# Kernel tuning notes

Hardware: AMD Instinct MI355X
Metric: run time of the kernel (lower is better)

Reference implementation:

```python
import jax, jax.numpy as jnp
import numpy as np

HIDDEN = 2048
HEAD_DIM = 128
N_HEADS = 16
N_KV_HEADS = 8
Q_DIM = N_HEADS * HEAD_DIM          # 2048
K_DIM = N_KV_HEADS * HEAD_DIM       # 1024
ROPE_THETA = 1.0e6
EPS = 1e-6
T = 4096


def setup_inputs() -> dict:
    key = jax.random.key(0)
    ks = jax.random.split(key, 4)
    x = jax.random.normal(ks[0], (T, HIDDEN), dtype=jnp.float32)
    qkv_w = jax.random.normal(ks[1], (Q_DIM + 2 * K_DIM, HIDDEN), dtype=jnp.float32) * 0.02
    o_w = jax.random.normal(ks[2], (HIDDEN, Q_DIM), dtype=jnp.float32) * 0.02
    q_norm_w = jnp.ones((HEAD_DIM,), dtype=jnp.float32)
    k_norm_w = jnp.ones((HEAD_DIM,), dtype=jnp.float32)
    positions = jnp.arange(T, dtype=jnp.int64 if jax.config.jax_enable_x64 else jnp.int32)
    return {"x": x, "qkv_w": qkv_w, "q_norm_w": q_norm_w,
            "k_norm_w": k_norm_w, "o_w": o_w, "positions": positions}


def _rms_norm(v, w):
    # v: [T, H, D]; normalize over last dim
    var = jnp.mean(v * v, axis=-1, keepdims=True)
    return v * jax.lax.rsqrt(var + EPS) * w


def _rope(v, cos, sin):
    # neox style: rotate halves. v: [T, H, D]; cos/sin: [T, 1, D/2]
    half = v.shape[-1] // 2
    v1, v2 = v[..., :half], v[..., half:]
    return jnp.concatenate([v1 * cos - v2 * sin, v2 * cos + v1 * sin], axis=-1)


def reference(x, qkv_w, q_norm_w, k_norm_w, o_w, positions):
    t = x.shape[0]
    qkv = x @ qkv_w.T                                   # [T, Q_DIM+2*K_DIM]
    q = qkv[:, :Q_DIM].reshape(t, N_HEADS, HEAD_DIM)
    k = qkv[:, Q_DIM:Q_DIM + K_DIM].reshape(t, N_KV_HEADS, HEAD_DIM)
    v = qkv[:, Q_DIM + K_DIM:].reshape(t, N_KV_HEADS, HEAD_DIM)

    q = _rms_norm(q, q_norm_w)
    k = _rms_norm(k, k_norm_w)

    half = HEAD_DIM // 2
    inv_freq = 1.0 / (ROPE_THETA ** (jnp.arange(0, half, dtype=jnp.float32) / half))
    freqs = positions.astype(jnp.float32)[:, None] * inv_freq[None, :]  # [T, half]
    cos = jnp.cos(freqs)[:, None, :]                     # [T, 1, half]
    sin = jnp.sin(freqs)[:, None, :]
    q = _rope(q, cos, sin)
    k = _rope(k, cos, sin)

    # GQA: each kv head serves N_HEADS // N_KV_HEADS query heads
    rep = N_HEADS // N_KV_HEADS
    k = jnp.repeat(k, rep, axis=1)                       # [T, N_HEADS, D]
    v = jnp.repeat(v, rep, axis=1)

    scale = 1.0 / np.sqrt(HEAD_DIM)
    scores = jnp.einsum('thd,shd->hts', q, k) * scale    # [H, T, T]
    causal = positions[:, None] >= positions[None, :]    # [T, T]
    scores = jnp.where(causal[None, :, :], scores, jnp.float32(-1e9))
    attn = jax.nn.softmax(scores, axis=-1)
    o = jnp.einsum('hts,shd->thd', attn, v)              # [T, H, D]
    o = o.reshape(t, Q_DIM)
    return o @ o_w.T                                     # [T, HIDDEN]
```

## Files before the change

### kernel.cpp

```cpp
#include <hip/hip_runtime.h>

#define Tq   4096
#define HIDN 2048
#define NHEAD 16
#define NKV  8
#define DH   128
#define QKVN 4096

typedef unsigned short u16;
typedef unsigned int   u32;
typedef __attribute__((ext_vector_type(8))) __bf16 bf16x8;
typedef __attribute__((ext_vector_type(8))) u16    u16x8;
typedef __attribute__((ext_vector_type(4))) float  f32x4;

#define GLD16(gp, lp) __builtin_amdgcn_global_load_lds( \
    (const __attribute__((address_space(1))) void*)(gp), \
    (__attribute__((address_space(3))) void*)(lp), 16, 0, 0)

__device__ __forceinline__ u16 f2bf(float f) {
  union { float f; u32 u; } v; v.f = f;
  return (u16)((v.u + 0x7fffu + ((v.u >> 16) & 1u)) >> 16);
}
__device__ __forceinline__ float bf2f(u32 bits) {
  union { u32 u; float f; } v; v.u = bits << 16;
  return v.f;
}

__global__ __launch_bounds__(256) void cast_bf16_kernel(const float* __restrict__ in,
                                                        u16* __restrict__ out, int n) {
  int i = (blockIdx.x * 256 + threadIdx.x) * 8;
  if (i >= n) return;
  f32x4 a = *(const f32x4*)(in + i);
  f32x4 b = *(const f32x4*)(in + i + 4);
  u16x8 o;
  #pragma unroll
  for (int j = 0; j < 4; ++j) { o[j] = f2bf(a[j]); o[4 + j] = f2bf(b[j]); }
  *(u16x8*)(out + i) = o;
}

template<bool OUT_BF16>
__global__ __launch_bounds__(256) void gemm_bt_kernel(const u16* __restrict__ A,
                                                      const u16* __restrict__ B,
                                                      void* __restrict__ Cout,
                                                      int M, int N, int K) {
  __shared__ u16 As[128 * 32];
  __shared__ u16 Bs[128 * 32];
  const int tid = threadIdx.x;
  const int lane = tid & 63, wv = tid >> 6;
  const int wr = wv >> 1, wc = wv & 1;
  const int g = lane >> 4, c = lane & 15;
  const int nbn = N >> 7;
  const int bm = blockIdx.x / nbn, bn = blockIdx.x % nbn;
  const int m0 = bm << 7, n0 = bn << 7;

  const int srow = tid >> 2;
  const int sk8 = (tid & 3) * 8;
  const u16* gA0 = A + (size_t)(m0 + srow) * K + sk8;
  const u16* gA1 = gA0 + (size_t)64 * K;
  const u16* gB0 = B + (size_t)(n0 + srow) * K + sk8;
  const u16* gB1 = gB0 + (size_t)64 * K;
  u16* lA0 = As + (wv * 64) * 8;
  u16* lA1 = As + (wv * 64 + 256) * 8;
  u16* lB0 = Bs + (wv * 64) * 8;
  u16* lB1 = Bs + (wv * 64 + 256) * 8;

  f32x4 acc[4][4] = {};

  for (int kt = 0; kt < K; kt += 32) {
    __syncthreads();
    GLD16(gA0 + kt, lA0); GLD16(gA1 + kt, lA1);
    GLD16(gB0 + kt, lB0); GLD16(gB1 + kt, lB1);
    __syncthreads();
    bf16x8 af[4], bfr[4];
    #pragma unroll
    for (int mi = 0; mi < 4; ++mi)
      af[mi] = *(const bf16x8*)&As[(wr * 64 + mi * 16 + c) * 32 + g * 8];
    #pragma unroll
    for (int ni = 0; ni < 4; ++ni)
      bfr[ni] = *(const bf16x8*)&Bs[(wc * 64 + ni * 16 + c) * 32 + g * 8];
    #pragma unroll
    for (int mi = 0; mi < 4; ++mi)
      #pragma unroll
      for (int ni = 0; ni < 4; ++ni)
        acc[mi][ni] = __builtin_amdgcn_mfma_f32_16x16x32_bf16(af[mi], bfr[ni], acc[mi][ni], 0, 0, 0);
  }

  #pragma unroll
  for (int mi = 0; mi < 4; ++mi)
    #pragma unroll
    for (int ni = 0; ni < 4; ++ni) {
      const int row = m0 + wr * 64 + mi * 16 + 4 * g;
      const int col = n0 + wc * 64 + ni * 16 + c;
      #pragma unroll
      for (int j = 0; j < 4; ++j) {
        if (OUT_BF16) ((u16*)Cout)[(size_t)(row + j) * N + col] = f2bf(acc[mi][ni][j]);
        else          ((float*)Cout)[(size_t)(row + j) * N + col] = acc[mi][ni][j];
      }
    }
}

__global__ __launch_bounds__(256) void normrope_kernel(u16* __restrict__ qkv,
                                                       const float* __restrict__ qw,
                                                       const float* __restrict__ kw) {
  const int tid = threadIdx.x, lane = tid & 63, wv = tid >> 6;
  const int wid = blockIdx.x * 4 + wv;
  const int t = wid / 24;
  const int hh = wid % 24;
  const int off = (hh < 16) ? hh * DH : 2048 + (hh - 16) * DH;
  const float* w = (hh < 16) ? qw : kw;
  u16* base = qkv + (size_t)t * QKVN + off;
  const int d0 = lane * 2;

  u32 raw = *(const u32*)(base + d0);
  float v0 = bf2f(raw & 0xffffu), v1 = bf2f(raw >> 16);
  float ss = v0 * v0 + v1 * v1;
  #pragma unroll
  for (int m = 1; m <= 32; m <<= 1) ss += __shfl_xor(ss, m);
  const float rn = rsqrtf(ss * (1.0f / 128.0f) + 1e-6f);
  float n0 = v0 * rn * w[d0];
  float n1 = v1 * rn * w[d0 + 1];
  float o0 = __shfl_xor(n0, 32);
  float o1 = __shfl_xor(n1, 32);
  const int j0 = (lane & 31) * 2;
  const float p = (float)t;
  const float lf = 0.31143075889568947f;
  float a0 = p * __builtin_exp2f(-lf * (float)j0);
  float a1 = p * __builtin_exp2f(-lf * (float)(j0 + 1));
  float c0 = cosf(a0), s0 = sinf(a0), c1 = cosf(a1), s1 = sinf(a1);
  float r0, r1;
  if (lane < 32) { r0 = n0 * c0 - o0 * s0; r1 = n1 * c1 - o1 * s1; }
  else           { r0 = n0 * c0 + o0 * s0; r1 = n1 * c1 + o1 * s1; }
  *(u32*)(base + d0) = (u32)f2bf(r0) | ((u32)f2bf(r1) << 16);
}

__global__ __launch_bounds__(256) void vtrans_kernel(const u16* __restrict__ qkv,
                                                     u16* __restrict__ vt) {
  __shared__ u16 tile[64][72];
  const int tid = threadIdx.x;
  const int b = blockIdx.x;
  const int kvh = b >> 7;
  const int r = b & 127;
  const int t0 = (r & 63) * 64;
  const int d0 = (r >> 6) * 64;
  #pragma unroll
  for (int i = 0; i < 2; ++i) {
    int cidx = tid + i * 256;
    int trow = cidx >> 3, dcol = (cidx & 7) * 8;
    u16x8 v = *(const u16x8*)&qkv[(size_t)(t0 + trow) * QKVN + 3072 + kvh * DH + d0 + dcol];
    *(u16x8*)&tile[trow][dcol] = v;
  }
  __syncthreads();
  #pragma unroll
  for (int i = 0; i < 2; ++i) {
    int cidx = tid + i * 256;
    int drow = cidx >> 3, tcol = (cidx & 7) * 8;
    u16x8 v;
    #pragma unroll
    for (int j = 0; j < 8; ++j) v[j] = tile[tcol + j][drow];
    *(u16x8*)&vt[(size_t)kvh * DH * Tq + (size_t)(d0 + drow) * Tq + t0 + tcol] = v;
  }
}

__global__ __launch_bounds__(256) void attn5_kernel(const u16* __restrict__ qkv,
                                                    const u16* __restrict__ vt,
                                                    u16* __restrict__ o) {
  __shared__ u16 Ks[64 * 128];
  __shared__ u16 Vs[144 * 64];
  __shared__ u16 Ps[4][2][16][72];
  const int tid = threadIdx.x, lane = tid & 63, wv = tid >> 6;
  const int g = lane >> 4, c = lane & 15;
  const int bid = blockIdx.x;
  const int head = bid & 15;
  const int qt = 31 - (bid >> 4);
  const int kvh = head >> 1;
  const float c2 = 0.08838834764831845f * 1.4426950408889634f;
  const float THR = 40.0f;
  const int xk = c & 7;

  for (int i = tid; i < 16 * 64; i += 256) Vs[128 * 64 + i] = (i < 64) ? 0x3F80 : 0;

  int kOff[4], kDst[4], vOff[4], vDst[4];
  #pragma unroll
  for (int j = 0; j < 4; ++j) {
    int i = j * 256 + tid;
    int kr = i >> 4, kcc = i & 15;
    kOff[j] = kr * QKVN + 2048 + kvh * DH + kcc * 8;
    kDst[j] = kr * 128 + ((kcc ^ (kr & 7)) * 8);
    int vr = i >> 3, vcc = i & 7;
    vOff[j] = vr * Tq + vcc * 8;
    vDst[j] = vr * 64 + ((vcc ^ (vr & 7)) * 8);
  }
  const u16* vkv = vt + (size_t)kvh * DH * Tq;
  u16x8 kreg[4], vreg[4];

  const int q0w = qt * 128 + wv * 32;
  const int nkvb = qt * 2 + 2;

  bf16x8 qf[2][4];
  #pragma unroll
  for (int r = 0; r < 2; ++r)
    #pragma unroll
    for (int ks = 0; ks < 4; ++ks)
      qf[r][ks] = *(const bf16x8*)&qkv[(size_t)(q0w + r * 16 + c) * QKVN + head * DH + ks * 32 + g * 8];

  f32x4 oacc[2][9] = {};
  float mrow[2][4] = {{ -3e38f, -3e38f, -3e38f, -3e38f },
                      { -3e38f, -3e38f, -3e38f, -3e38f }};

  #pragma unroll
  for (int j = 0; j < 4; ++j) {
    kreg[j] = *(const u16x8*)(qkv + kOff[j]);
    vreg[j] = *(const u16x8*)(vkv + vOff[j]);
  }

  for (int kb = 0; kb < nkvb; ++kb) {
    const int kv0 = kb * 64;
    #pragma unroll
    for (int j = 0; j < 4; ++j) {
      *(u16x8*)&Ks[kDst[j]] = kreg[j];
      *(u16x8*)&Vs[vDst[j]] = vreg[j];
    }
    __syncthreads();
    {
      const int kvn = (kb + 1 < nkvb) ? (kv0 + 64) : kv0;
      #pragma unroll
      for (int j = 0; j < 4; ++j) {
        kreg[j] = *(const u16x8*)(qkv + (size_t)kvn * QKVN + kOff[j]);
        vreg[j] = *(const u16x8*)(vkv + kvn + vOff[j]);
      }
    }
    if (kv0 <= q0w + 31) {
      f32x4 s[2][4] = {};
      #pragma unroll
      for (int st = 0; st < 4; ++st)
        #pragma unroll
        for (int ks = 0; ks < 4; ++ks) {
          bf16x8 kf = *(const bf16x8*)&Ks[(st * 16 + c) * 128 + (((ks * 4 + g) ^ xk) * 8)];
          s[0][st] = __builtin_amdgcn_mfma_f32_16x16x32_bf16(qf[0][ks], kf, s[0][st], 0, 0, 0);
          s[1][st] = __builtin_amdgcn_mfma_f32_16x16x32_bf16(qf[1][ks], kf, s[1][st], 0, 0, 0);
        }
      if (kv0 + 63 > q0w) {
        #pragma unroll
        for (int r = 0; r < 2; ++r)
          #pragma unroll
          for (int st = 0; st < 4; ++st) {
            const int kvc = kv0 + st * 16 + c;
            #pragma unroll
            for (int j = 0; j < 4; ++j)
              if (kvc > q0w + r * 16 + 4 * g + j) s[r][st][j] = -1e9f;
          }
      }
      float mx[2][4];
      int need = 0;
      #pragma unroll
      for (int r = 0; r < 2; ++r)
        #pragma unroll
        for (int j = 0; j < 4; ++j) {
          float m3 = fmaxf(fmaxf(s[r][0][j], s[r][1][j]), fmaxf(s[r][2][j], s[r][3][j]));
          m3 = fmaxf(m3, __shfl_xor(m3, 1));
          m3 = fmaxf(m3, __shfl_xor(m3, 2));
          m3 = fmaxf(m3, __shfl_xor(m3, 4));
          m3 = fmaxf(m3, __shfl_xor(m3, 8));
          mx[r][j] = m3;
          need |= (m3 > mrow[r][j] + THR);
        }
      if (__any(need)) {
        #pragma unroll
        for (int r = 0; r < 2; ++r)
          #pragma unroll
          for (int j = 0; j < 4; ++j) {
            const float mn = fmaxf(mrow[r][j], mx[r][j]);
            const float alpha = __builtin_exp2f(c2 * (mrow[r][j] - mn));
            mrow[r][j] = mn;
            #pragma unroll
            for (int db = 0; db < 9; ++db) oacc[r][db][j] *= alpha;
          }
      }
      #pragma unroll
      for (int r = 0; r < 2; ++r) {
        #pragma unroll
        for (int j = 0; j < 4; ++j) {
          const float cm = c2 * mrow[r][j];
          #pragma unroll
          for (int st = 0; st < 4; ++st)
            s[r][st][j] = __builtin_exp2f(c2 * s[r][st][j] - cm);
        }
        #pragma unroll
        for (int st = 0; st < 4; ++st) {
          u32 pk01, pk23;
          asm("v_cvt_pk_bf16_f32 %0, %1, %2" : "=v"(pk01) : "v"(s[r][st][0]), "v"(s[r][st][1]));
          asm("v_cvt_pk_bf16_f32 %0, %1, %2" : "=v"(pk23) : "v"(s[r][st][2]), "v"(s[r][st][3]));
          Ps[wv][r][4 * g + 0][st * 16 + c] = (u16)pk01;
          Ps[wv][r][4 * g + 1][st * 16 + c] = (u16)(pk01 >> 16);
          Ps[wv][r][4 * g + 2][st * 16 + c] = (u16)pk23;
          Ps[wv][r][4 * g + 3][st * 16 + c] = (u16)(pk23 >> 16);
        }
      }
      bf16x8 pa[2][2];
      #pragma unroll
      for (int r = 0; r < 2; ++r) {
        pa[r][0] = *(const bf16x8*)&Ps[wv][r][c][g * 8];
        pa[r][1] = *(const bf16x8*)&Ps[wv][r][c][32 + g * 8];
      }
      #pragma unroll
      for (int db = 0; db < 9; ++db) {
        bf16x8 vf0 = *(const bf16x8*)&Vs[(db * 16 + c) * 64 + ((g ^ xk) * 8)];
        oacc[0][db] = __builtin_amdgcn_mfma_f32_16x16x32_bf16(pa[0][0], vf0, oacc[0][db], 0, 0, 0);
        oacc[1][db] = __builtin_amdgcn_mfma_f32_16x16x32_bf16(pa[1][0], vf0, oacc[1][db], 0, 0, 0);
        bf16x8 vf1 = *(const bf16x8*)&Vs[(db * 16 + c) * 64 + (((4 + g) ^ xk) * 8)];
        oacc[0][db] = __builtin_amdgcn_mfma_f32_16x16x32_bf16(pa[0][1], vf1, oacc[0][db], 0, 0, 0);
        oacc[1][db] = __builtin_amdgcn_mfma_f32_16x16x32_bf16(pa[1][1], vf1, oacc[1][db], 0, 0, 0);
      }
    }
    __syncthreads();
  }

  #pragma unroll
  for (int r = 0; r < 2; ++r)
    #pragma unroll
    for (int j = 0; j < 4; ++j) {
      const float ls = __shfl(oacc[r][8][j], lane & 48);
      const float inv = 1.0f / ls;
      #pragma unroll
      for (int db = 0; db < 8; ++db)
        o[(size_t)(q0w + r * 16 + 4 * g + j) * HIDN + head * DH + db * 16 + c] =
            f2bf(oacc[r][db][j] * inv);
    }
}

extern "C" void kernel_launch(void* const* d_in, const int* in_sizes, int n_in,
                              void* d_out, int out_size, void* d_ws, size_t ws_size,
                              hipStream_t stream) {
  const float* x    = (const float*)d_in[0];
  const float* qkvw = (const float*)d_in[1];
  const float* qnw  = (const float*)d_in[2];
  const float* knw  = (const float*)d_in[3];
  const float* ow   = (const float*)d_in[4];

  char* ws = (char*)d_ws;
  u16* xb   = (u16*)ws;
  u16* wb   = (u16*)(ws + (16u << 20));
  u16* qkvb = (u16*)(ws + (32u << 20));
  u16* vtb  = (u16*)(ws + (64u << 20));
  u16* owb  = xb;
  u16* ob   = wb;

  cast_bf16_kernel<<<4096, 256, 0, stream>>>(x,    xb, Tq * HIDN);
  cast_bf16_kernel<<<4096, 256, 0, stream>>>(qkvw, wb, QKVN * HIDN);
  gemm_bt_kernel<true><<<1024, 256, 0, stream>>>(xb, wb, (void*)qkvb, Tq, QKVN, HIDN);
  normrope_kernel<<<24576, 256, 0, stream>>>(qkvb, qnw, knw);
  vtrans_kernel<<<1024, 256, 0, stream>>>(qkvb, vtb);
  cast_bf16_kernel<<<2048, 256, 0, stream>>>(ow, owb, HIDN * HIDN);
  attn5_kernel<<<512, 256, 0, stream>>>(qkvb, vtb, ob);
  gemm_bt_kernel<false><<<512, 256, 0, stream>>>(ob, owb, d_out, Tq, HIDN, HIDN);
}
```

Baseline: 509.9 us.

## Pair causal q-tiles per block and double-buffer K/V with direct-to-LDS loads

Each block now handles two q-tiles, p and 31-p, so every block does the same amount of causal work, and the grid shrinks from 512 to 256 blocks. K/V tiles are streamed with global_load_lds into double-buffered shared memory, replacing register staging, and the XOR swizzle moves onto the global addresses. MFMA sections are wrapped in s_setprio to favour matrix issue. The cost is doubled LDS use, which may lower occupancy, and a grid of 256 blocks that may underfill the CUs.

```diff
diff --git a/kernel.cpp b/kernel.cpp
--- a/kernel.cpp
+++ b/kernel.cpp
@@ -161,41 +161,39 @@
   }
 }
 
-__global__ __launch_bounds__(256) void attn5_kernel(const u16* __restrict__ qkv,
+__global__ __launch_bounds__(256) void attn6_kernel(const u16* __restrict__ qkv,
                                                     const u16* __restrict__ vt,
                                                     u16* __restrict__ o) {
-  __shared__ u16 Ks[64 * 128];
-  __shared__ u16 Vs[144 * 64];
+  __shared__ u16 Ks[2][64 * 128];
+  __shared__ u16 Vs[2][128 * 64];
+  __shared__ u16 Vones[16 * 64];
   __shared__ u16 Ps[4][2][16][72];
   const int tid = threadIdx.x, lane = tid & 63, wv = tid >> 6;
   const int g = lane >> 4, c = lane & 15;
   const int bid = blockIdx.x;
-  const int head = bid & 15;
-  const int qt = 31 - (bid >> 4);
-  const int kvh = head >> 1;
+  const int kvh = bid & 7;
+  const int rest = bid >> 3;
+  const int head = 2 * kvh + (rest & 1);
+  const int p = rest >> 1;
   const float c2 = 0.08838834764831845f * 1.4426950408889634f;
   const float THR = 40.0f;
   const int xk = c & 7;
 
-  for (int i = tid; i < 16 * 64; i += 256) Vs[128 * 64 + i] = (i < 64) ? 0x3F80 : 0;
-
-  int kOff[4], kDst[4], vOff[4], vDst[4];
+  for (int i = tid; i < 16 * 64; i += 256) Vones[i] = (i < 64) ? 0x3F80 : 0;
+
+  int kOff[4], vOff[4];
   #pragma unroll
   for (int j = 0; j < 4; ++j) {
     int i = j * 256 + tid;
     int kr = i >> 4, kcc = i & 15;
-    kOff[j] = kr * QKVN + 2048 + kvh * DH + kcc * 8;
-    kDst[j] = kr * 128 + ((kcc ^ (kr & 7)) * 8);
+    kOff[j] = kr * QKVN + 2048 + kvh * DH + ((kcc ^ (kr & 7)) * 8);
     int vr = i >> 3, vcc = i & 7;
-    vOff[j] = vr * Tq + vcc * 8;
-    vDst[j] = vr * 64 + ((vcc ^ (vr & 7)) * 8);
+    vOff[j] = vr * Tq + ((vcc ^ (vr & 7)) * 8);
   }
   const u16* vkv = vt + (size_t)kvh * DH * Tq;
-  u16x8 kreg[4], vreg[4];
-
-  const int q0w = qt * 128 + wv * 32;
-  const int nkvb = qt * 2 + 2;
-
+
+  int qt = p;
+  int q0w = qt * 128 + wv * 32;
   bf16x8 qf[2][4];
   #pragma unroll
   for (int r = 0; r < 2; ++r)
@@ -207,38 +205,75 @@
   float mrow[2][4] = {{ -3e38f, -3e38f, -3e38f, -3e38f },
                       { -3e38f, -3e38f, -3e38f, -3e38f }};
 
+  asm volatile("s_waitcnt lgkmcnt(0)" ::: "memory");
   #pragma unroll
   for (int j = 0; j < 4; ++j) {
-    kreg[j] = *(const u16x8*)(qkv + kOff[j]);
-    vreg[j] = *(const u16x8*)(vkv + vOff[j]);
-  }
-
-  for (int kb = 0; kb < nkvb; ++kb) {
-    const int kv0 = kb * 64;
-    #pragma unroll
-    for (int j = 0; j < 4; ++j) {
-      *(u16x8*)&Ks[kDst[j]] = kreg[j];
-      *(u16x8*)&Vs[vDst[j]] = vreg[j];
-    }
-    __syncthreads();
-    {
-      const int kvn = (kb + 1 < nkvb) ? (kv0 + 64) : kv0;
+    GLD16(qkv + kOff[j], &Ks[0][(j * 256 + wv * 64) * 8]);
+    GLD16(vkv + vOff[j], &Vs[0][(j * 256 + wv * 64) * 8]);
+  }
+
+  const int bnd = 2 * p + 2;
+  #pragma unroll 1
+  for (int ph = 0; ph <= 65; ++ph) {
+    const int cur = ph & 1;
+    const int kv0 = (ph < bnd) ? ph * 64 : (ph - bnd) * 64;
+    if (ph < 65) {
+      const int phn = ph + 1;
+      const int nxt = (phn < bnd) ? phn * 64 : (phn - bnd) * 64;
+      const u16* kb_ = qkv + (size_t)nxt * QKVN;
+      const u16* vb_ = vkv + nxt;
       #pragma unroll
       for (int j = 0; j < 4; ++j) {
-        kreg[j] = *(const u16x8*)(qkv + (size_t)kvn * QKVN + kOff[j]);
-        vreg[j] = *(const u16x8*)(vkv + kvn + vOff[j]);
-      }
-    }
+        GLD16(kb_ + kOff[j], &Ks[cur ^ 1][(j * 256 + wv * 64) * 8]);
+        GLD16(vb_ + vOff[j], &Vs[cur ^ 1][(j * 256 + wv * 64) * 8]);
+      }
+      asm volatile("s_waitcnt vmcnt(8)" ::: "memory");
+    } else {
+      asm volatile("s_waitcnt vmcnt(0)" ::: "memory");
+    }
+    __builtin_amdgcn_s_barrier();
+    asm volatile("" ::: "memory");
+
+    if (ph == bnd) {
+      #pragma unroll
+      for (int r = 0; r < 2; ++r)
+        #pragma unroll
+        for (int j = 0; j < 4; ++j) {
+          const float ls = __shfl(oacc[r][8][j], lane & 48);
+          const float inv = 1.0f / ls;
+          #pragma unroll
+          for (int db = 0; db < 8; ++db)
+            o[(size_t)(q0w + r * 16 + 4 * g + j) * HIDN + head * DH + db * 16 + c] =
+                f2bf(oacc[r][db][j] * inv);
+        }
+      qt = 31 - p;
+      q0w = qt * 128 + wv * 32;
+      #pragma unroll
+      for (int r = 0; r < 2; ++r)
+        #pragma unroll
+        for (int ks = 0; ks < 4; ++ks)
+          qf[r][ks] = *(const bf16x8*)&qkv[(size_t)(q0w + r * 16 + c) * QKVN + head * DH + ks * 32 + g * 8];
+      #pragma unroll
+      for (int r = 0; r < 2; ++r) {
+        #pragma unroll
+        for (int db = 0; db < 9; ++db) oacc[r][db] = (f32x4){0.f, 0.f, 0.f, 0.f};
+        #pragma unroll
+        for (int j = 0; j < 4; ++j) mrow[r][j] = -3e38f;
+      }
+    }
+
     if (kv0 <= q0w + 31) {
       f32x4 s[2][4] = {};
+      __builtin_amdgcn_s_setprio(1);
       #pragma unroll
       for (int st = 0; st < 4; ++st)
         #pragma unroll
         for (int ks = 0; ks < 4; ++ks) {
-          bf16x8 kf = *(const bf16x8*)&Ks[(st * 16 + c) * 128 + (((ks * 4 + g) ^ xk) * 8)];
+          bf16x8 kf = *(const bf16x8*)&Ks[cur][(st * 16 + c) * 128 + (((ks * 4 + g) ^ xk) * 8)];
           s[0][st] = __builtin_amdgcn_mfma_f32_16x16x32_bf16(qf[0][ks], kf, s[0][st], 0, 0, 0);
           s[1][st] = __builtin_amdgcn_mfma_f32_16x16x32_bf16(qf[1][ks], kf, s[1][st], 0, 0, 0);
         }
+      __builtin_amdgcn_s_setprio(0);
       if (kv0 + 63 > q0w) {
         #pragma unroll
         for (int r = 0; r < 2; ++r)
@@ -302,17 +337,23 @@
         pa[r][0] = *(const bf16x8*)&Ps[wv][r][c][g * 8];
         pa[r][1] = *(const bf16x8*)&Ps[wv][r][c][32 + g * 8];
       }
+      __builtin_amdgcn_s_setprio(1);
       #pragma unroll
       for (int db = 0; db < 9; ++db) {
-        bf16x8 vf0 = *(const bf16x8*)&Vs[(db * 16 + c) * 64 + ((g ^ xk) * 8)];
+        const u16* vrow = (db < 8) ? &Vs[cur][(db * 16 + c) * 64] : &Vones[c * 64];
+        bf16x8 vf0 = *(const bf16x8*)&vrow[(g ^ xk) * 8];
         oacc[0][db] = __builtin_amdgcn_mfma_f32_16x16x32_bf16(pa[0][0], vf0, oacc[0][db], 0, 0, 0);
         oacc[1][db] = __builtin_amdgcn_mfma_f32_16x16x32_bf16(pa[1][0], vf0, oacc[1][db], 0, 0, 0);
-        bf16x8 vf1 = *(const bf16x8*)&Vs[(db * 16 + c) * 64 + (((4 + g) ^ xk) * 8)];
+        bf16x8 vf1 = *(const bf16x8*)&vrow[((4 + g) ^ xk) * 8];
         oacc[0][db] = __builtin_amdgcn_mfma_f32_16x16x32_bf16(pa[0][1], vf1, oacc[0][db], 0, 0, 0);
         oacc[1][db] = __builtin_amdgcn_mfma_f32_16x16x32_bf16(pa[1][1], vf1, oacc[1][db], 0, 0, 0);
       }
-    }
-    __syncthreads();
+      __builtin_amdgcn_s_setprio(0);
+    }
+    asm volatile("s_waitcnt lgkmcnt(0)" ::: "memory");
+    __builtin_amdgcn_sched_barrier(0);
+    __builtin_amdgcn_s_barrier();
+    asm volatile("" ::: "memory");
   }
 
   #pragma unroll
@@ -351,6 +392,6 @@
   normrope_kernel<<<24576, 256, 0, stream>>>(qkvb, qnw, knw);
   vtrans_kernel<<<1024, 256, 0, stream>>>(qkvb, vtb);
   cast_bf16_kernel<<<2048, 256, 0, stream>>>(ow, owb, HIDN * HIDN);
-  attn5_kernel<<<512, 256, 0, stream>>>(qkvb, vtb, ob);
+  attn6_kernel<<<256, 256, 0, stream>>>(qkvb, vtb, ob);
   gemm_bt_kernel<false><<<512, 256, 0, stream>>>(ob, owb, d_out, Tq, HIDN, HIDN);
 }
```

Result: no change. 519.4 us (+1.9%).

## Load attention K/V tiles directly to LDS and remap blocks for locality

Applied to the files above, without the earlier changes.

The attention kernel now stages K and V tiles with global_load_lds, folding the XOR swizzle into the source offsets, instead of prefetching them through registers. This trades the old register-prefetch overlap for lower register pressure, and launch_bounds(256,2) asks for two blocks per CU. The block-to-head mapping changes so that blocks sharing a KV head are grouped. MFMA sections are bracketed with s_setprio, and the GEMM gets an XCD-style block swizzle for cache locality. The risk is losing the explicit overlap between loading the next tile and computing the current one, which now depends on occupancy alone.

```diff
diff --git a/kernel.cpp b/kernel.cpp
--- a/kernel.cpp
+++ b/kernel.cpp
@@ -50,7 +50,9 @@
   const int wr = wv >> 1, wc = wv & 1;
   const int g = lane >> 4, c = lane & 15;
   const int nbn = N >> 7;
-  const int bm = blockIdx.x / nbn, bn = blockIdx.x % nbn;
+  const int cpx = gridDim.x >> 3;
+  const int swz = (blockIdx.x & 7) * cpx + (blockIdx.x >> 3);
+  const int bm = swz / nbn, bn = swz % nbn;
   const int m0 = bm << 7, n0 = bn << 7;
 
   const int srow = tid >> 2;
@@ -161,37 +163,36 @@
   }
 }
 
-__global__ __launch_bounds__(256) void attn5_kernel(const u16* __restrict__ qkv,
-                                                    const u16* __restrict__ vt,
-                                                    u16* __restrict__ o) {
+__global__ __launch_bounds__(256, 2) void attn7_kernel(const u16* __restrict__ qkv,
+                                                       const u16* __restrict__ vt,
+                                                       u16* __restrict__ o) {
   __shared__ u16 Ks[64 * 128];
-  __shared__ u16 Vs[144 * 64];
+  __shared__ u16 Vs[128 * 64];
+  __shared__ u16 Vones[16 * 64];
   __shared__ u16 Ps[4][2][16][72];
   const int tid = threadIdx.x, lane = tid & 63, wv = tid >> 6;
   const int g = lane >> 4, c = lane & 15;
   const int bid = blockIdx.x;
-  const int head = bid & 15;
-  const int qt = 31 - (bid >> 4);
-  const int kvh = head >> 1;
+  const int kvh = bid & 7;
+  const int rest = bid >> 3;
+  const int head = 2 * kvh + (rest & 1);
+  const int qt = 31 - (rest >> 1);
   const float c2 = 0.08838834764831845f * 1.4426950408889634f;
   const float THR = 40.0f;
   const int xk = c & 7;
 
-  for (int i = tid; i < 16 * 64; i += 256) Vs[128 * 64 + i] = (i < 64) ? 0x3F80 : 0;
-
-  int kOff[4], kDst[4], vOff[4], vDst[4];
+  for (int i = tid; i < 16 * 64; i += 256) Vones[i] = (i < 64) ? 0x3F80 : 0;
+
+  int kOff[4], vOff[4];
   #pragma unroll
   for (int j = 0; j < 4; ++j) {
     int i = j * 256 + tid;
     int kr = i >> 4, kcc = i & 15;
-    kOff[j] = kr * QKVN + 2048 + kvh * DH + kcc * 8;
-    kDst[j] = kr * 128 + ((kcc ^ (kr & 7)) * 8);
+    kOff[j] = kr * QKVN + 2048 + kvh * DH + ((kcc ^ (kr & 7)) * 8);
     int vr = i >> 3, vcc = i & 7;
-    vOff[j] = vr * Tq + vcc * 8;
-    vDst[j] = vr * 64 + ((vcc ^ (vr & 7)) * 8);
+    vOff[j] = vr * Tq + ((vcc ^ (vr & 7)) * 8);
   }
   const u16* vkv = vt + (size_t)kvh * DH * Tq;
-  u16x8 kreg[4], vreg[4];
 
   const int q0w = qt * 128 + wv * 32;
   const int nkvb = qt * 2 + 2;
@@ -207,30 +208,19 @@
   float mrow[2][4] = {{ -3e38f, -3e38f, -3e38f, -3e38f },
                       { -3e38f, -3e38f, -3e38f, -3e38f }};
 
-  #pragma unroll
-  for (int j = 0; j < 4; ++j) {
-    kreg[j] = *(const u16x8*)(qkv + kOff[j]);
-    vreg[j] = *(const u16x8*)(vkv + vOff[j]);
-  }
-
+  #pragma unroll 1
   for (int kb = 0; kb < nkvb; ++kb) {
     const int kv0 = kb * 64;
+    __syncthreads();
     #pragma unroll
     for (int j = 0; j < 4; ++j) {
-      *(u16x8*)&Ks[kDst[j]] = kreg[j];
-      *(u16x8*)&Vs[vDst[j]] = vreg[j];
+      GLD16(qkv + (size_t)kv0 * QKVN + kOff[j], &Ks[(j * 256 + wv * 64) * 8]);
+      GLD16(vkv + kv0 + vOff[j],               &Vs[(j * 256 + wv * 64) * 8]);
     }
     __syncthreads();
-    {
-      const int kvn = (kb + 1 < nkvb) ? (kv0 + 64) : kv0;
-      #pragma unroll
-      for (int j = 0; j < 4; ++j) {
-        kreg[j] = *(const u16x8*)(qkv + (size_t)kvn * QKVN + kOff[j]);
-        vreg[j] = *(const u16x8*)(vkv + kvn + vOff[j]);
-      }
-    }
     if (kv0 <= q0w + 31) {
       f32x4 s[2][4] = {};
+      __builtin_amdgcn_s_setprio(1);
       #pragma unroll
       for (int st = 0; st < 4; ++st)
         #pragma unroll
@@ -239,6 +229,7 @@
           s[0][st] = __builtin_amdgcn_mfma_f32_16x16x32_bf16(qf[0][ks], kf, s[0][st], 0, 0, 0);
           s[1][st] = __builtin_amdgcn_mfma_f32_16x16x32_bf16(qf[1][ks], kf, s[1][st], 0, 0, 0);
         }
+      __builtin_amdgcn_s_setprio(0);
       if (kv0 + 63 > q0w) {
         #pragma unroll
         for (int r = 0; r < 2; ++r)
@@ -302,17 +293,19 @@
         pa[r][0] = *(const bf16x8*)&Ps[wv][r][c][g * 8];
         pa[r][1] = *(const bf16x8*)&Ps[wv][r][c][32 + g * 8];
       }
+      __builtin_amdgcn_s_setprio(1);
       #pragma unroll
       for (int db = 0; db < 9; ++db) {
-        bf16x8 vf0 = *(const bf16x8*)&Vs[(db * 16 + c) * 64 + ((g ^ xk) * 8)];
+        const u16* vrow = (db < 8) ? &Vs[(db * 16 + c) * 64] : &Vones[c * 64];
+        bf16x8 vf0 = *(const bf16x8*)&vrow[(g ^ xk) * 8];
         oacc[0][db] = __builtin_amdgcn_mfma_f32_16x16x32_bf16(pa[0][0], vf0, oacc[0][db], 0, 0, 0);
         oacc[1][db] = __builtin_amdgcn_mfma_f32_16x16x32_bf16(pa[1][0], vf0, oacc[1][db], 0, 0, 0);
-        bf16x8 vf1 = *(const bf16x8*)&Vs[(db * 16 + c) * 64 + (((4 + g) ^ xk) * 8)];
+        bf16x8 vf1 = *(const bf16x8*)&vrow[((4 + g) ^ xk) * 8];
         oacc[0][db] = __builtin_amdgcn_mfma_f32_16x16x32_bf16(pa[0][1], vf1, oacc[0][db], 0, 0, 0);
         oacc[1][db] = __builtin_amdgcn_mfma_f32_16x16x32_bf16(pa[1][1], vf1, oacc[1][db], 0, 0, 0);
       }
+      __builtin_amdgcn_s_setprio(0);
     }
-    __syncthreads();
   }
 
   #pragma unroll
@@ -351,6 +344,6 @@
   normrope_kernel<<<24576, 256, 0, stream>>>(qkvb, qnw, knw);
   vtrans_kernel<<<1024, 256, 0, stream>>>(qkvb, vtb);
   cast_bf16_kernel<<<2048, 256, 0, stream>>>(ow, owb, HIDN * HIDN);
-  attn5_kernel<<<512, 256, 0, stream>>>(qkvb, vtb, ob);
+  attn7_kernel<<<512, 256, 0, stream>>>(qkvb, vtb, ob);
   gemm_bt_kernel<false><<<512, 256, 0, stream>>>(ob, owb, d_out, Tq, HIDN, HIDN);
 }
```

Result: faster. 498.3 us (-2.3%).
